# Kernel tuning notes

Measured on AMD Instinct MI355X. Metric: run time of the kernel, lower is better.

Reference implementation:

```python
import jax, jax.numpy as jnp
import numpy as np

B, T, C = 4, 2048, 768
H = 12
D = C // H  # head dim 64

def setup_inputs() -> dict:
    key = jax.random.key(0)
    ks = jax.random.split(key, 6)
    scale = 1.0 / np.sqrt(C)
    x = jax.random.normal(ks[0], (B, T, C), dtype=jnp.float32)
    attention_mask = jax.random.randint(ks[1], (B, T), 0, 2, dtype=jnp.int64)
    Wqkv = jax.random.normal(ks[2], (C, 3 * C), dtype=jnp.float32) * scale
    bqkv = jax.random.normal(ks[3], (3 * C,), dtype=jnp.float32) * 0.02
    Wo = jax.random.normal(ks[4], (C, C), dtype=jnp.float32) * scale
    bo = jax.random.normal(ks[5], (C,), dtype=jnp.float32) * 0.02
    return {"x": x, "attention_mask": attention_mask, "Wqkv": Wqkv,
            "bqkv": bqkv, "Wo": Wo, "bo": bo}

def reference(x, attention_mask, Wqkv, bqkv, Wo, bo):
    # fused QKV projection: [B,T,3C]
    qkv = jnp.einsum('btc,cd->btd', x, Wqkv) + bqkv
    q, k, v = jnp.split(qkv, 3, axis=-1)
    # reshape to [B,H,T,D]
    q = q.reshape(B, T, H, D).transpose(0, 2, 1, 3)
    k = k.reshape(B, T, H, D).transpose(0, 2, 1, 3)
    v = v.reshape(B, T, H, D).transpose(0, 2, 1, 3)
    # module quirk: True (attended) where attention_mask == 0
    keep = (attention_mask == 0)[:, None, None, :]  # [B,1,1,T]
    scores = jnp.einsum('bhqd,bhkd->bhqk', q, k) / np.sqrt(D)
    scores = jnp.where(keep, scores, jnp.finfo(scores.dtype).min)
    probs = jax.nn.softmax(scores, axis=-1)
    context = jnp.einsum('bhqk,bhkd->bhqd', probs, v)
    context = context.transpose(0, 2, 1, 3).reshape(B, T, C)
    return jnp.einsum('btc,cd->btd', context, Wo) + bo
```

## Files before the change

### kernel.cpp

```cpp
#include <hip/hip_runtime.h>
#include <stdint.h>

#define AS1 __attribute__((address_space(1)))
#define AS3 __attribute__((address_space(3)))

typedef _Float16 f16;
typedef _Float16 f16x8 __attribute__((ext_vector_type(8)));
typedef _Float16 f16x4 __attribute__((ext_vector_type(4)));
typedef _Float16 f16x2 __attribute__((ext_vector_type(2)));
typedef float    f32x4  __attribute__((ext_vector_type(4)));
typedef float    f32x16 __attribute__((ext_vector_type(16)));

#define B_  4
#define T_  2048
#define C_  768
#define H_  12
#define D_  64
#define M_  (B_*T_)
#define N1_ (3*C_)

__device__ __forceinline__ void g2l16(const void* g, void* l) {
  __builtin_amdgcn_global_load_lds((const AS1 void*)g, (AS3 void*)l, 16, 0, 0);
}

__device__ __forceinline__ f32x4 fzero4() { f32x4 z = {0.f, 0.f, 0.f, 0.f}; return z; }

__device__ __forceinline__ f16x2 pk_f16(float a, float b) {
  auto t = __builtin_amdgcn_cvt_pkrtz(a, b);
  return *(f16x2*)&t;
}

__global__ __launch_bounds__(256)
void transpose_cvt_k(const float* __restrict__ in, f16* __restrict__ out, int R, int C) {
  __shared__ float tile[32][33];
  const int tx = threadIdx.x & 31, ty = threadIdx.x >> 5;
  const int c0 = blockIdx.x * 32, r0 = blockIdx.y * 32;
#pragma unroll
  for (int i = 0; i < 32; i += 8)
    tile[ty + i][tx] = in[(long)(r0 + ty + i) * C + c0 + tx];
  __syncthreads();
#pragma unroll
  for (int i = 0; i < 32; i += 8)
    out[(long)(c0 + ty + i) * R + r0 + tx] = (f16)tile[tx][ty + i];
}

__global__ __launch_bounds__(256)
void convert_f32_f16(const float* __restrict__ in, f16* __restrict__ out) {
  const int i = (blockIdx.x * 256 + threadIdx.x) * 4;
  const float4 v = *(const float4*)(in + i);
  f16x4 o = {(f16)v.x, (f16)v.y, (f16)v.z, (f16)v.w};
  *(f16x4*)(out + i) = o;
}

__global__ __launch_bounds__(256)
void init_idx_kernel(int* __restrict__ idx, int* __restrict__ cnt) {
  const int g = blockIdx.x * 256 + threadIdx.x;
  idx[g] = 0;
  if (g < B_) cnt[g] = 0;
}

__global__ __launch_bounds__(256)
void compact_kernel(const int* __restrict__ mask, int* __restrict__ idx,
                    int* __restrict__ cnt) {
  const int b = blockIdx.y;
  const int t = blockIdx.x * 256 + threadIdx.x;
  if (mask[b * T_ + t] == 0) {
    const int s = atomicAdd(&cnt[b], 1);
    idx[b * T_ + s] = t;
  }
}

__global__ __launch_bounds__(256)
void build_vt(const f16* __restrict__ Vc, const int* __restrict__ cnt,
              f16* __restrict__ vt) {
  __shared__ f16 tile[32][33];
  const int z = blockIdx.z, b = z / H_, h = z % H_;
  const int s0 = blockIdx.x * 32, d0 = blockIdx.y * 32;
  if (s0 >= ((cnt[b] + 63) & ~63)) return;
  const int tx = threadIdx.x & 31, ty = threadIdx.x >> 5;
  f16* dst = vt + (long)z * D_ * T_;
#pragma unroll
  for (int i = 0; i < 32; i += 8)
    tile[ty + i][tx] = Vc[(long)(b * T_ + s0 + ty + i) * C_ + h * D_ + d0 + tx];
  __syncthreads();
#pragma unroll
  for (int i = 0; i < 32; i += 8)
    dst[(long)(d0 + ty + i) * T_ + s0 + tx] = tile[tx][ty + i];
}

template <typename OutT>
__global__ __launch_bounds__(256)
void gemm_bias_kernel(const f16* __restrict__ A, const f16* __restrict__ Bt,
                      const float* __restrict__ bias, OutT* __restrict__ Cc,
                      int K, int ldc) {
  __shared__ f16 lA[128 * 32];
  __shared__ f16 lB[128 * 32];
  const int tid = threadIdx.x;
  const int n0 = blockIdx.x * 128, m0 = blockIdx.y * 128;
  const int lane = tid & 63, w = tid >> 6;
  const int wm = (w & 1) * 64, wn = (w >> 1) * 64;
  const int r15 = lane & 15, q4 = lane >> 4;

  const int c0 = tid, c1 = 256 + tid;
  const int ar0 = c0 >> 2, ak0 = (c0 & 3) * 8;
  const int ar1 = c1 >> 2, ak1 = (c1 & 3) * 8;
  const f16* Ab = A + (long)m0 * K;
  const f16* Bb = Bt + (long)n0 * K;

  f32x4 acc[4][4];
#pragma unroll
  for (int i = 0; i < 4; i++)
#pragma unroll
    for (int j = 0; j < 4; j++) acc[i][j] = fzero4();

  for (int kb = 0; kb < K; kb += 32) {
    g2l16(Ab + (long)ar0 * K + kb + ak0, &lA[c0 * 8]);
    g2l16(Ab + (long)ar1 * K + kb + ak1, &lA[c1 * 8]);
    g2l16(Bb + (long)ar0 * K + kb + ak0, &lB[c0 * 8]);
    g2l16(Bb + (long)ar1 * K + kb + ak1, &lB[c1 * 8]);
    __syncthreads();
    f16x8 af[4], bfv[4];
#pragma unroll
    for (int mi = 0; mi < 4; mi++)
      af[mi] = *(const f16x8*)&lA[(wm + mi * 16 + r15) * 32 + q4 * 8];
#pragma unroll
    for (int ni = 0; ni < 4; ni++)
      bfv[ni] = *(const f16x8*)&lB[(wn + ni * 16 + r15) * 32 + q4 * 8];
#pragma unroll
    for (int mi = 0; mi < 4; mi++)
#pragma unroll
      for (int ni = 0; ni < 4; ni++)
        acc[mi][ni] = __builtin_amdgcn_mfma_f32_16x16x32_f16(af[mi], bfv[ni], acc[mi][ni], 0, 0, 0);
    __syncthreads();
  }

#pragma unroll
  for (int ni = 0; ni < 4; ni++) {
    const int col = n0 + wn + ni * 16 + r15;
    const float bs = bias[col];
#pragma unroll
    for (int mi = 0; mi < 4; mi++) {
#pragma unroll
      for (int r = 0; r < 4; r++) {
        const int row = m0 + wm + mi * 16 + q4 * 4 + r;
        Cc[(long)row * ldc + col] = (OutT)(acc[mi][ni][r] + bs);
      }
    }
  }
}

__global__ __launch_bounds__(256)
void gemm_qkv_kernel(const f16* __restrict__ A, const f16* __restrict__ Bt,
                     const float* __restrict__ bias, f16* __restrict__ Qb,
                     f16* __restrict__ Kc, f16* __restrict__ Vc,
                     const int* __restrict__ idx, const int* __restrict__ cnt) {
  const int K = C_;
  __shared__ f16 lA[128 * 32];
  __shared__ f16 lB[128 * 32];
  const int tid = threadIdx.x;
  const bool isQ = blockIdx.x < 6;
  const int n0 = (isQ ? blockIdx.x : blockIdx.x - 6) * 128;
  const int lane = tid & 63, w = tid >> 6;
  const int wm = (w & 1) * 64, wn = (w >> 1) * 64;
  const int r15 = lane & 15, q4 = lane >> 4;

  const int c0 = tid, c1 = 256 + tid;
  const int ar0 = c0 >> 2, ak0 = (c0 & 3) * 8;
  const int ar1 = c1 >> 2, ak1 = (c1 & 3) * 8;

  int b = 0, s0 = 0;
  long grow0, grow1;
  if (isQ) {
    const int m0 = blockIdx.y * 128;
    grow0 = m0 + ar0;
    grow1 = m0 + ar1;
  } else {
    b = blockIdx.y >> 4;
    s0 = (blockIdx.y & 15) * 128;
    if (s0 >= cnt[b]) return;
    const int* idx_b = idx + b * T_;
    grow0 = b * T_ + idx_b[s0 + ar0];
    grow1 = b * T_ + idx_b[s0 + ar1];
  }
  const f16* A0 = A + grow0 * K;
  const f16* A1 = A + grow1 * K;
  const f16* Bb = Bt + (long)((isQ ? 0 : C_) + n0) * K;

  f32x4 acc[4][4];
#pragma unroll
  for (int i = 0; i < 4; i++)
#pragma unroll
    for (int j = 0; j < 4; j++) acc[i][j] = fzero4();

  for (int kb = 0; kb < K; kb += 32) {
    g2l16(A0 + kb + ak0, &lA[c0 * 8]);
    g2l16(A1 + kb + ak1, &lA[c1 * 8]);
    g2l16(Bb + (long)ar0 * K + kb + ak0, &lB[c0 * 8]);
    g2l16(Bb + (long)ar1 * K + kb + ak1, &lB[c1 * 8]);
    __syncthreads();
    f16x8 af[4], bfv[4];
#pragma unroll
    for (int mi = 0; mi < 4; mi++)
      af[mi] = *(const f16x8*)&lA[(wm + mi * 16 + r15) * 32 + q4 * 8];
#pragma unroll
    for (int ni = 0; ni < 4; ni++)
      bfv[ni] = *(const f16x8*)&lB[(wn + ni * 16 + r15) * 32 + q4 * 8];
#pragma unroll
    for (int mi = 0; mi < 4; mi++)
#pragma unroll
      for (int ni = 0; ni < 4; ni++)
        acc[mi][ni] = __builtin_amdgcn_mfma_f32_16x16x32_f16(af[mi], bfv[ni], acc[mi][ni], 0, 0, 0);
    __syncthreads();
  }

#pragma unroll
  for (int ni = 0; ni < 4; ni++) {
    const int col = n0 + wn + ni * 16 + r15;
    const float bs = bias[isQ ? col : C_ + col];
    f16* outp;
    int ocol;
    if (isQ)            { outp = Qb; ocol = col; }
    else if (col < C_)  { outp = Kc; ocol = col; }
    else                { outp = Vc; ocol = col - C_; }
#pragma unroll
    for (int mi = 0; mi < 4; mi++) {
#pragma unroll
      for (int r = 0; r < 4; r++) {
        const int lrow = wm + mi * 16 + q4 * 4 + r;
        const long row = isQ ? (long)blockIdx.y * 128 + lrow
                             : (long)b * T_ + s0 + lrow;
        outp[row * C_ + ocol] = (f16)(acc[mi][ni][r] + bs);
      }
    }
  }
}

__global__ __launch_bounds__(256, 4)
void attn_kernel(const f16* __restrict__ Qb, const f16* __restrict__ Kc,
                 const f16* __restrict__ vtc, const int* __restrict__ cnt,
                 f16* __restrict__ ctx) {
  const int LDS_ = 72;
  __shared__ f16 QPs[128 * 72];
  __shared__ f16 Ks[64 * 72], Vs[64 * 72];
  const int tid = threadIdx.x, lane = tid & 63, w = tid >> 6;
  const int l31 = lane & 31, hh = lane >> 5;
  const int bh = blockIdx.y, b = bh / H_, h = bh % H_;
  const int q0 = blockIdx.x * 128;
  const f16* Qg = Qb + (long)(b * T_ + q0) * C_ + h * D_;
  const f16* Kbase = Kc + (long)b * T_ * C_ + h * D_;
  const f16* Vg = vtc + (long)bh * D_ * T_;
  const int nk = cnt[b];
  const int nkt = (nk + 63) >> 6;

  const f16 qsc = (f16)0.18033688f;
#pragma unroll
  for (int i = 0; i < 4; i++) {
    int c = i * 256 + tid, r = c >> 3, dcq = (c & 7) * 8;
    f16x8 v = *(const f16x8*)(Qg + (long)r * C_ + dcq);
#pragma unroll
    for (int j = 0; j < 8; j++) v[j] = v[j] * qsc;
    *(f16x8*)&QPs[r * LDS_ + dcq] = v;
  }
  __syncthreads();
  f16x8 bq[4];
#pragma unroll
  for (int j = 0; j < 4; j++)
    bq[j] = *(const f16x8*)&QPs[(w * 32 + l31) * LDS_ + j * 16 + hh * 8];

  const int r0 = tid >> 3, r1 = 32 + (tid >> 3), dc = (tid & 7) * 8;

  float l_acc = 0.f;
  f32x16 O[2];
#pragma unroll
  for (int dt = 0; dt < 2; dt++)
#pragma unroll
    for (int r = 0; r < 16; r++) O[dt][r] = 0.f;

  for (int kt = 0; kt < (nkt << 6); kt += 64) {
    __syncthreads();
    {
      f16x8 kv0 = *(const f16x8*)(Kbase + (long)(kt + r0) * C_ + dc);
      f16x8 kv1 = *(const f16x8*)(Kbase + (long)(kt + r1) * C_ + dc);
      f16x8 vv0 = *(const f16x8*)(Vg + (long)r0 * T_ + kt + dc);
      f16x8 vv1 = *(const f16x8*)(Vg + (long)r1 * T_ + kt + dc);
      *(f16x8*)&Ks[r0 * LDS_ + dc] = kv0;
      *(f16x8*)&Ks[r1 * LDS_ + dc] = kv1;
      *(f16x8*)&Vs[r0 * LDS_ + dc] = vv0;
      *(f16x8*)&Vs[r1 * LDS_ + dc] = vv1;
    }
    __syncthreads();

    const bool full = (kt + 64 <= nk);
#pragma unroll
    for (int ktile = 0; ktile < 2; ktile++) {
      f32x16 acc;
      if (full) {
#pragma unroll
        for (int r = 0; r < 16; r++) acc[r] = 0.f;
      } else {
        const int kbase = kt + ktile * 32 + hh * 4;
#pragma unroll
        for (int g = 0; g < 4; g++)
#pragma unroll
          for (int i = 0; i < 4; i++)
            acc[4 * g + i] = (kbase + 8 * g + i < nk) ? 0.f : -1e30f;
      }
#pragma unroll
      for (int j = 0; j < 4; j++) {
        f16x8 ak = *(const f16x8*)&Ks[(ktile * 32 + l31) * LDS_ + j * 16 + hh * 8];
        acc = __builtin_amdgcn_mfma_f32_32x32x16_f16(ak, bq[j], acc, 0, 0, 0);
      }
#pragma unroll
      for (int g = 0; g < 4; g++) {
        const float p0 = __builtin_amdgcn_exp2f(acc[4 * g + 0]);
        const float p1 = __builtin_amdgcn_exp2f(acc[4 * g + 1]);
        const float p2 = __builtin_amdgcn_exp2f(acc[4 * g + 2]);
        const float p3 = __builtin_amdgcn_exp2f(acc[4 * g + 3]);
        l_acc += (p0 + p1) + (p2 + p3);
        const f16x2 lo = pk_f16(p0, p1), hi = pk_f16(p2, p3);
        f16x4 pv; pv[0] = lo[0]; pv[1] = lo[1]; pv[2] = hi[0]; pv[3] = hi[1];
        *(f16x4*)&QPs[(w * 32 + l31) * LDS_ + ktile * 32 + g * 8 + hh * 4] = pv;
      }
    }
    asm volatile("s_waitcnt lgkmcnt(0)" ::: "memory");

#pragma unroll
    for (int j = 0; j < 4; j++) {
      f16x8 pa = *(const f16x8*)&QPs[(w * 32 + l31) * LDS_ + j * 16 + hh * 8];
#pragma unroll
      for (int dt = 0; dt < 2; dt++) {
        f16x8 vb = *(const f16x8*)&Vs[(dt * 32 + l31) * LDS_ + j * 16 + hh * 8];
        O[dt] = __builtin_amdgcn_mfma_f32_32x32x16_f16(pa, vb, O[dt], 0, 0, 0);
      }
    }
  }

  l_acc += __shfl_xor(l_acc, 32);
  float* Lw = (float*)&QPs[(w * 32) * LDS_];
  asm volatile("s_waitcnt lgkmcnt(0)" ::: "memory");
  if (hh == 0) Lw[l31] = l_acc;
  asm volatile("s_waitcnt lgkmcnt(0)" ::: "memory");
#pragma unroll
  for (int g = 0; g < 4; g++) {
    const f32x4 lv = *(const f32x4*)&Lw[g * 8 + hh * 4];
#pragma unroll
    for (int i = 0; i < 4; i++) {
      const float inv = 1.f / lv[i];
      const int row = b * T_ + q0 + w * 32 + g * 8 + hh * 4 + i;
#pragma unroll
      for (int dt = 0; dt < 2; dt++)
        ctx[(long)row * C_ + h * D_ + dt * 32 + l31] = (f16)(O[dt][4 * g + i] * inv);
    }
  }
}

extern "C" void kernel_launch(void* const* d_in, const int* in_sizes, int n_in,
                              void* d_out, int out_size, void* d_ws, size_t ws_size,
                              hipStream_t stream) {
  (void)in_sizes; (void)n_in; (void)out_size; (void)ws_size;
  const float* x    = (const float*)d_in[0];
  const int*   mask = (const int*)  d_in[1];
  const float* Wqkv = (const float*)d_in[2];
  const float* bqkv = (const float*)d_in[3];
  const float* Wo   = (const float*)d_in[4];
  const float* bo   = (const float*)d_in[5];
  float* out = (float*)d_out;

  char* ws = (char*)d_ws;
  const size_t OFF_WQKVT = 0;
  const size_t OFF_WOT   = OFF_WQKVT + 3538944;
  const size_t OFF_Q     = OFF_WOT + 1179648;
  const size_t OFF_KC    = OFF_Q + 12582912;
  const size_t OFF_VC    = OFF_KC + 12582912;
  const size_t OFF_VT    = OFF_VC + 12582912;
  const size_t OFF_XH    = OFF_VT + 12582912;
  const size_t OFF_IDX   = OFF_XH + 12582912;
  const size_t OFF_CNT   = OFF_IDX + 32768;
  f16* WqkvT = (f16*)(ws + OFF_WQKVT);
  f16* WoT   = (f16*)(ws + OFF_WOT);
  f16* Qb    = (f16*)(ws + OFF_Q);
  f16* Kc    = (f16*)(ws + OFF_KC);
  f16* Vc    = (f16*)(ws + OFF_VC);
  f16* Vtc   = (f16*)(ws + OFF_VT);
  f16* xh    = (f16*)(ws + OFF_XH);
  f16* ctx   = (f16*)(ws + OFF_XH);
  int* idx   = (int*)(ws + OFF_IDX);
  int* cnt   = (int*)(ws + OFF_CNT);

  transpose_cvt_k<<<dim3(72, 24), 256, 0, stream>>>(Wqkv, WqkvT, 768, 2304);
  transpose_cvt_k<<<dim3(24, 24), 256, 0, stream>>>(Wo, WoT, 768, 768);
  convert_f32_f16<<<dim3(M_ * C_ / 1024), 256, 0, stream>>>(x, xh);
  init_idx_kernel<<<dim3(B_ * T_ / 256), 256, 0, stream>>>(idx, cnt);
  compact_kernel<<<dim3(T_ / 256, B_), 256, 0, stream>>>(mask, idx, cnt);
  gemm_qkv_kernel<<<dim3(18, 64), 256, 0, stream>>>(xh, WqkvT, bqkv, Qb, Kc, Vc, idx, cnt);
  build_vt<<<dim3(64, 2, 48), 256, 0, stream>>>(Vc, cnt, Vtc);
  attn_kernel<<<dim3(16, 48), 256, 0, stream>>>(Qb, Kc, Vtc, cnt, ctx);
  gemm_bias_kernel<float><<<dim3(6, 64), 256, 0, stream>>>(ctx, WoT, bo, out, 768, 768);
}
```

Baseline: 206.5 us.

## Use 256x256 tiles with double-buffered swizzled LDS in QKV GEMM

Rewrites the QKV projection GEMM to use 256x256 output tiles with 512 threads and a K-step of 64. LDS is now double-buffered, so loads of the next k-tile overlap MFMA work on the current one, and an XOR swizzle is meant to avoid bank conflicts. Larger tiles raise data reuse and cut the number of barriers. The risks are a smaller grid (9x32 blocks) that may leave CUs idle on this part, higher register pressure from 32 accumulators per thread, and 128KB of LDS per block, which limits occupancy.

```diff
diff --git a/kernel.cpp b/kernel.cpp
--- a/kernel.cpp
+++ b/kernel.cpp
@@ -149,86 +149,112 @@
   }
 }
 
-__global__ __launch_bounds__(256)
-void gemm_qkv_kernel(const f16* __restrict__ A, const f16* __restrict__ Bt,
-                     const float* __restrict__ bias, f16* __restrict__ Qb,
-                     f16* __restrict__ Kc, f16* __restrict__ Vc,
-                     const int* __restrict__ idx, const int* __restrict__ cnt) {
+__global__ __launch_bounds__(512, 2)
+void gemm_qkv256(const f16* __restrict__ A, const f16* __restrict__ Bt,
+                 const float* __restrict__ bias, f16* __restrict__ Qb,
+                 f16* __restrict__ Kc, f16* __restrict__ Vc,
+                 const int* __restrict__ idx, const int* __restrict__ cnt) {
   const int K = C_;
-  __shared__ f16 lA[128 * 32];
-  __shared__ f16 lB[128 * 32];
+  __shared__ f16 lA[2 * 256 * 64];
+  __shared__ f16 lB[2 * 256 * 64];
   const int tid = threadIdx.x;
-  const bool isQ = blockIdx.x < 6;
-  const int n0 = (isQ ? blockIdx.x : blockIdx.x - 6) * 128;
+  const int nb = blockIdx.x;
+  const int mb = blockIdx.y;
+  const bool isQ = nb < 3;
+
+  int b = 0, s0 = 0;
+  if (!isQ) {
+    b = mb >> 3;
+    s0 = (mb & 7) * 256;
+    if (s0 >= cnt[b]) return;
+  }
+
   const int lane = tid & 63, w = tid >> 6;
-  const int wm = (w & 1) * 64, wn = (w >> 1) * 64;
+  const int wmi = w >> 2, wni = w & 3;
   const int r15 = lane & 15, q4 = lane >> 4;
-
-  const int c0 = tid, c1 = 256 + tid;
-  const int ar0 = c0 >> 2, ak0 = (c0 & 3) * 8;
-  const int ar1 = c1 >> 2, ak1 = (c1 & 3) * 8;
-
-  int b = 0, s0 = 0;
-  long grow0, grow1;
-  if (isQ) {
-    const int m0 = blockIdx.y * 128;
-    grow0 = m0 + ar0;
-    grow1 = m0 + ar1;
-  } else {
-    b = blockIdx.y >> 4;
-    s0 = (blockIdx.y & 15) * 128;
-    if (s0 >= cnt[b]) return;
-    const int* idx_b = idx + b * T_;
-    grow0 = b * T_ + idx_b[s0 + ar0];
-    grow1 = b * T_ + idx_b[s0 + ar1];
-  }
-  const f16* A0 = A + grow0 * K;
-  const f16* A1 = A + grow1 * K;
-  const f16* Bb = Bt + (long)((isQ ? 0 : C_) + n0) * K;
-
-  f32x4 acc[4][4];
-#pragma unroll
-  for (int i = 0; i < 4; i++)
+  const int rx = (r15 & 7) * 8;
+
+  const int trow = tid >> 3;
+  const int koffsw = (((tid & 7) ^ (trow & 7)) * 8);
+  const f16* pA[4];
+  const f16* pB[4];
+#pragma unroll
+  for (int i = 0; i < 4; i++) {
+    const int ri = i * 64 + trow;
+    long grow;
+    if (isQ) grow = (long)mb * 256 + ri;
+    else     grow = (long)b * T_ + idx[b * T_ + s0 + ri];
+    pA[i] = A + grow * K + koffsw;
+    pB[i] = Bt + (long)(nb * 256 + ri) * K + koffsw;
+  }
+  const int lofs = tid * 8;
+
+  f32x4 acc[8][4];
+#pragma unroll
+  for (int i = 0; i < 8; i++)
 #pragma unroll
     for (int j = 0; j < 4; j++) acc[i][j] = fzero4();
 
-  for (int kb = 0; kb < K; kb += 32) {
-    g2l16(A0 + kb + ak0, &lA[c0 * 8]);
-    g2l16(A1 + kb + ak1, &lA[c1 * 8]);
-    g2l16(Bb + (long)ar0 * K + kb + ak0, &lB[c0 * 8]);
-    g2l16(Bb + (long)ar1 * K + kb + ak1, &lB[c1 * 8]);
+#define STAGE_QKV(bufsel, kb) do {                                        \
+  const int lb = (bufsel) * 16384;                                        \
+  _Pragma("unroll")                                                       \
+  for (int i = 0; i < 4; i++) {                                           \
+    g2l16(pA[i] + (kb), &lA[lb + i * 4096 + lofs]);                       \
+    g2l16(pB[i] + (kb), &lB[lb + i * 4096 + lofs]);                       \
+  }                                                                       \
+} while (0)
+
+#define COMPUTE_QKV(bufsel) do {                                          \
+  const int lb = (bufsel) * 16384;                                        \
+  _Pragma("unroll")                                                       \
+  for (int kh = 0; kh < 2; kh++) {                                        \
+    const int cofs = (kh * 32 + q4 * 8) ^ rx;                             \
+    f16x8 af[8], bf[4];                                                   \
+    _Pragma("unroll")                                                     \
+    for (int mi = 0; mi < 8; mi++)                                        \
+      af[mi] = *(const f16x8*)&lA[lb + (wmi * 128 + mi * 16 + r15) * 64 + cofs]; \
+    _Pragma("unroll")                                                     \
+    for (int ni = 0; ni < 4; ni++)                                        \
+      bf[ni] = *(const f16x8*)&lB[lb + (wni * 64 + ni * 16 + r15) * 64 + cofs];  \
+    _Pragma("unroll")                                                     \
+    for (int mi = 0; mi < 8; mi++)                                        \
+      _Pragma("unroll")                                                   \
+      for (int ni = 0; ni < 4; ni++)                                      \
+        acc[mi][ni] = __builtin_amdgcn_mfma_f32_16x16x32_f16(af[mi], bf[ni], acc[mi][ni], 0, 0, 0); \
+  }                                                                       \
+} while (0)
+
+  STAGE_QKV(0, 0);
+  __syncthreads();
+
+  int cur = 0;
+  const int NT = K / 64;
+  for (int t = 0; t < NT - 1; t++) {
+    STAGE_QKV(cur ^ 1, (t + 1) * 64);
+    COMPUTE_QKV(cur);
     __syncthreads();
-    f16x8 af[4], bfv[4];
-#pragma unroll
-    for (int mi = 0; mi < 4; mi++)
-      af[mi] = *(const f16x8*)&lA[(wm + mi * 16 + r15) * 32 + q4 * 8];
-#pragma unroll
-    for (int ni = 0; ni < 4; ni++)
-      bfv[ni] = *(const f16x8*)&lB[(wn + ni * 16 + r15) * 32 + q4 * 8];
-#pragma unroll
-    for (int mi = 0; mi < 4; mi++)
-#pragma unroll
-      for (int ni = 0; ni < 4; ni++)
-        acc[mi][ni] = __builtin_amdgcn_mfma_f32_16x16x32_f16(af[mi], bfv[ni], acc[mi][ni], 0, 0, 0);
-    __syncthreads();
-  }
+    cur ^= 1;
+  }
+  COMPUTE_QKV(cur);
+
+#undef STAGE_QKV
+#undef COMPUTE_QKV
 
 #pragma unroll
   for (int ni = 0; ni < 4; ni++) {
-    const int col = n0 + wn + ni * 16 + r15;
-    const float bs = bias[isQ ? col : C_ + col];
+    const int cN = nb * 256 + wni * 64 + ni * 16 + r15;
+    const float bs = bias[cN];
     f16* outp;
     int ocol;
-    if (isQ)            { outp = Qb; ocol = col; }
-    else if (col < C_)  { outp = Kc; ocol = col; }
-    else                { outp = Vc; ocol = col - C_; }
-#pragma unroll
-    for (int mi = 0; mi < 4; mi++) {
+    long rowbase;
+    if (isQ)               { outp = Qb; ocol = cN;        rowbase = (long)mb * 256; }
+    else if (cN < 2 * C_)  { outp = Kc; ocol = cN - C_;   rowbase = (long)b * T_ + s0; }
+    else                   { outp = Vc; ocol = cN - 2*C_; rowbase = (long)b * T_ + s0; }
+#pragma unroll
+    for (int mi = 0; mi < 8; mi++) {
 #pragma unroll
       for (int r = 0; r < 4; r++) {
-        const int lrow = wm + mi * 16 + q4 * 4 + r;
-        const long row = isQ ? (long)blockIdx.y * 128 + lrow
-                             : (long)b * T_ + s0 + lrow;
+        const long row = rowbase + wmi * 128 + mi * 16 + q4 * 4 + r;
         outp[row * C_ + ocol] = (f16)(acc[mi][ni][r] + bs);
       }
     }
@@ -392,7 +418,7 @@
   convert_f32_f16<<<dim3(M_ * C_ / 1024), 256, 0, stream>>>(x, xh);
   init_idx_kernel<<<dim3(B_ * T_ / 256), 256, 0, stream>>>(idx, cnt);
   compact_kernel<<<dim3(T_ / 256, B_), 256, 0, stream>>>(mask, idx, cnt);
-  gemm_qkv_kernel<<<dim3(18, 64), 256, 0, stream>>>(xh, WqkvT, bqkv, Qb, Kc, Vc, idx, cnt);
+  gemm_qkv256<<<dim3(9, 32), 512, 0, stream>>>(xh, WqkvT, bqkv, Qb, Kc, Vc, idx, cnt);
   build_vt<<<dim3(64, 2, 48), 256, 0, stream>>>(Vc, cnt, Vtc);
   attn_kernel<<<dim3(16, 48), 256, 0, stream>>>(Qb, Kc, Vtc, cnt, ctx);
   gemm_bias_kernel<float><<<dim3(6, 64), 256, 0, stream>>>(ctx, WoT, bo, out, 768, 768);
```

New measurement: 201.1 us. 1.03x faster.
